# Kernel tuning notes

Hardware: AMD Instinct MI355X
Metric: run time of the kernel (lower is better)

The kernel has to match this reference:

```python
import jax, jax.numpy as jnp
import numpy as np
from jax import lax

FIR_TAPS = np.array([1.0, 3.0, 3.0, 1.0], dtype=np.float32)
FACTOR = 2
GAIN = 1.0


def _fir_kernel(C):
    # _setup_kernel: outer product, normalize to sum 1; upsample scales by gain*factor**2
    k = np.outer(FIR_TAPS, FIR_TAPS)
    k = k / k.sum() * (GAIN * FACTOR ** 2)  # 4x4 kernel, sum == 4
    k = jnp.asarray(k, jnp.float32)
    return jnp.tile(k[None, None], (C, 1, 1, 1))  # [C,1,4,4] depthwise


def setup_inputs() -> dict:
    key = jax.random.key(0)
    k1, k2, k3 = jax.random.split(key, 3)
    x = jax.random.normal(k1, (16, 256, 64, 64), jnp.float32)
    W = jax.random.normal(k2, (256, 256, 3, 3), jnp.float32) * 0.02
    b = jax.random.normal(k3, (256,), jnp.float32) * 0.02
    return {"x": x, "W": W, "b": b}


def reference(x, W, b):
    B, C, H, Wd = x.shape
    kern = _fir_kernel(C)
    # upfirdn2d upsample: zero-insert by 2 (lhs_dilation), pad0=2 / pad1=1(+up-1=2),
    # depthwise FIR correlation -> [B, C, 2H, 2W]
    p0, p1 = 2, 2  # pad1 = p//2 + (factor-1) trailing zeros folded into padding
    h = lax.conv_general_dilated(
        x, kern, window_strides=(1, 1), padding=((p0, p1), (p0, p1)),
        lhs_dilation=(FACTOR, FACTOR),
        dimension_numbers=("NCHW", "OIHW", "NCHW"), feature_group_count=C)
    # 3x3 conv, padding=1, stride=1 -> [B, out_ch, 2H, 2W]
    y = lax.conv_general_dilated(
        h, W, window_strides=(1, 1), padding=((1, 1), (1, 1)),
        dimension_numbers=("NCHW", "OIHW", "NCHW"))
    return y + b[None, :, None, None]
```

## Files before the change

### kernel.cpp

```cpp
#include <hip/hip_runtime.h>
#include <hip/hip_bf16.h>
#include <stdint.h>

typedef __attribute__((ext_vector_type(8))) short bf16x8;
typedef __attribute__((ext_vector_type(4))) float f32x4;

#define PH 130
#define NT 36
#define ITERS 18

__device__ __forceinline__ short f2bf(float f) {
  uint32_t u = __builtin_bit_cast(uint32_t, f);
  u = (u + 0x7FFFu + ((u >> 16) & 1u)) >> 16;
  return (short)u;
}

__device__ __forceinline__ void gload16(const void* g, void* l) {
  __builtin_amdgcn_global_load_lds(
      (const __attribute__((address_space(1))) void*)g,
      (__attribute__((address_space(3))) void*)l, 16, 0, 0);
}

__global__ void wpack(const float* __restrict__ W, short* __restrict__ A) {
  int tid = blockIdx.x * 256 + threadIdx.x;
  if (tid >= 256 * 2304) return;
  int co = tid / 2304;
  int r  = tid - co * 2304;
  int tap = r >> 8, ci = r & 255;
  A[tid] = f2bf(W[((size_t)(co * 256 + ci)) * 9 + tap]);
}

__global__ void fir_up(const float* __restrict__ x, short* __restrict__ hT) {
  const int bp = blockIdx.x;
  const int b = bp / PH, pp = bp - b * PH;
  const int ci0 = blockIdx.y << 6;
  const int t = threadIdx.x;
  short* outrow = hT + ((size_t)(b * PH + pp) * PH) * 256 + ci0;

  if (pp == 0 || pp == PH - 1) {
    for (int idx = t; idx < PH * 64; idx += 256) {
      int qp = idx >> 6, c = idx & 63;
      outrow[(size_t)qp * 256 + c] = 0;
    }
    return;
  }
  const int p = pp - 1;
  int i0, i1; float wr0, wr1;
  if (!(p & 1)) { i0 = (p >> 1) - 1; i1 = p >> 1;     wr0 = 0.25f; wr1 = 0.75f; }
  else          { i0 = p >> 1;       i1 = (p >> 1)+1; wr0 = 0.75f; wr1 = 0.25f; }

  __shared__ float X[2][64][65];
#pragma unroll
  for (int r = 0; r < 2; ++r) {
    int ir = r ? i1 : i0;
    bool ok = (ir >= 0 && ir < 64);
#pragma unroll
    for (int it = 0; it < 4; ++it) {
      int idx = it * 256 + t;
      int ci = idx >> 4, jq = idx & 15;
      f32x4 v = {0.f, 0.f, 0.f, 0.f};
      if (ok)
        v = *(const f32x4*)&x[((size_t)(b * 256 + ci0 + ci) * 64 + ir) * 64 + jq * 4];
      X[r][jq * 4 + 0][ci] = v[0];
      X[r][jq * 4 + 1][ci] = v[1];
      X[r][jq * 4 + 2][ci] = v[2];
      X[r][jq * 4 + 3][ci] = v[3];
    }
  }
  __syncthreads();

  const int c = t & 63;
  for (int qp = (t >> 6); qp < PH; qp += 4) {
    float val = 0.f;
    if (qp >= 1 && qp <= 128) {
      int q = qp - 1;
      int j0, j1; float wc0, wc1;
      if (!(q & 1)) { j0 = (q >> 1) - 1; j1 = q >> 1; wc0 = 0.25f; wc1 = 0.75f; }
      else          { j0 = q >> 1;       j1 = j0 + 1; wc0 = 0.75f; wc1 = 0.25f; }
      float v00 = (j0 >= 0) ? X[0][j0][c] : 0.f;
      float v10 = (j0 >= 0) ? X[1][j0][c] : 0.f;
      float v01 = (j1 < 64) ? X[0][j1][c] : 0.f;
      float v11 = (j1 < 64) ? X[1][j1][c] : 0.f;
      val = wr0 * (wc0 * v00 + wc1 * v01) + wr1 * (wc0 * v10 + wc1 * v11);
    }
    outrow[(size_t)qp * 256 + c] = f2bf(val);
  }
}

__global__ __launch_bounds__(512) void conv3x3_gemm(
    const short* __restrict__ hT, const short* __restrict__ Wp,
    const float* __restrict__ bias, float* __restrict__ y) {
  __shared__ short ldsA[2][16384];
  __shared__ short ldsB[2][16384];
  const int tid = threadIdx.x;
  const int lane = tid & 63, w = tid >> 6;
  const int wm = w >> 2, wn = w & 3;

  const int bid = blockIdx.x;
  const int jblk = (bid & 7) * 32 + (bid >> 3);

  int aRow[4], aKk[4];
  const short* srcB[4];
#pragma unroll
  for (int h = 0; h < 2; ++h)
#pragma unroll
    for (int i = 0; i < 2; ++i) {
      int o = h * 16384 + i * 8192 + w * 1024 + lane * 16;
      int L = o ^ (((o >> 7) & 7) << 4);
      int row = L >> 7, kk = (L & 127) >> 1;
      aRow[h * 2 + i] = row; aKk[h * 2 + i] = kk;
      srcB[h * 2 + i] = Wp + (size_t)row * 2304 + kk;
    }

  int aP[2], bP[2];
#pragma unroll
  for (int ks = 0; ks < 2; ++ks) {
    int La = (wm * 128 + (lane & 15)) * 128 + (lane >> 4) * 16 + ks * 64;
    aP[ks] = La ^ ((lane & 7) << 4);
    int Lb = (wn * 64 + (lane & 15)) * 128 + (lane >> 4) * 16 + ks * 64;
    bP[ks] = Lb ^ ((lane & 7) << 4);
  }

  const char* LA0 = (const char*)&ldsA[0][0];
  const char* LB0 = (const char*)&ldsB[0][0];
  const char* LA1 = (const char*)&ldsA[1][0];
  const char* LB1 = (const char*)&ldsB[1][0];

  for (int mi = 0; mi < 4; ++mi) {
    const int tau = jblk * 4 + mi;
    const int b = tau >> 6, p0 = (tau & 63) * 2;

    const short* srcA[4];
#pragma unroll
    for (int j = 0; j < 4; ++j)
      srcA[j] = hT + ((size_t)((b * PH + p0 + (aRow[j] >> 7)) * PH + (aRow[j] & 127))) * 256 + aKk[j];

    auto offA = [&](int t) {
      int tap = t >> 2, ci0 = (t & 3) << 6;
      int dm = (tap >= 6) ? 2 : (tap >= 3) ? 1 : 0;
      int dn = tap - 3 * dm;
      return (dm * PH + dn) * 256 + ci0;
    };
    auto offB = [&](int t) { return (t >> 2) * 256 + ((t & 3) << 6); };

    auto stageA = [&](int t, int h) {
      int o = offA(t);
      short* dst = &ldsA[t & 1][h * 8192];
#pragma unroll
      for (int i = 0; i < 2; ++i)
        gload16(srcA[h * 2 + i] + o, dst + i * 4096 + w * 512);
    };
    auto stageB = [&](int t, int h) {
      int o = offB(t);
      short* dst = &ldsB[t & 1][h * 8192];
#pragma unroll
      for (int i = 0; i < 2; ++i)
        gload16(srcB[h * 2 + i] + o, dst + i * 4096 + w * 512);
    };

    stageA(0, 0); stageB(0, 0); stageB(0, 1); stageA(0, 1);
    stageA(1, 0); stageB(1, 0); stageB(1, 1);
    asm volatile("s_waitcnt vmcnt(6)" ::: "memory");
    __builtin_amdgcn_s_barrier();

    f32x4 acc[8][4];
#pragma unroll
    for (int m = 0; m < 8; ++m)
#pragma unroll
      for (int n = 0; n < 4; ++n) acc[m][n] = (f32x4){0.f, 0.f, 0.f, 0.f};

    for (int i = 0; i < ITERS; ++i) {
      const int u = 2 * i, v = u + 1;
      const bool more = (u + 2 < NT);
      bf16x8 a_[2][4], c_[2][4], b_[2][2], b2[2][2];

#pragma unroll
      for (int ks = 0; ks < 2; ++ks) {
#pragma unroll
        for (int m = 0; m < 4; ++m) a_[ks][m] = *(const bf16x8*)(LA0 + aP[ks] + m * 2048);
#pragma unroll
        for (int n = 0; n < 2; ++n) b_[ks][n] = *(const bf16x8*)(LB0 + bP[ks] + n * 2048);
      }
      stageA(v, 1);
      asm volatile("s_waitcnt lgkmcnt(8)" ::: "memory");
      __builtin_amdgcn_s_barrier();
      asm volatile("s_waitcnt lgkmcnt(0)" ::: "memory");
      __builtin_amdgcn_s_setprio(1);
#pragma unroll
      for (int m = 0; m < 4; ++m)
#pragma unroll
        for (int n = 0; n < 2; ++n) {
          acc[m][n] = __builtin_amdgcn_mfma_f32_16x16x32_bf16(a_[0][m], b_[0][n], acc[m][n], 0, 0, 0);
          acc[m][n] = __builtin_amdgcn_mfma_f32_16x16x32_bf16(a_[1][m], b_[1][n], acc[m][n], 0, 0, 0);
        }
      __builtin_amdgcn_s_setprio(0);
      __builtin_amdgcn_s_barrier();

#pragma unroll
      for (int ks = 0; ks < 2; ++ks)
#pragma unroll
        for (int n = 0; n < 2; ++n) b2[ks][n] = *(const bf16x8*)(LB0 + bP[ks] + (n + 2) * 2048);
      __builtin_amdgcn_s_barrier();
      asm volatile("s_waitcnt lgkmcnt(0)" ::: "memory");
      __builtin_amdgcn_s_setprio(1);
#pragma unroll
      for (int m = 0; m < 4; ++m)
#pragma unroll
        for (int n = 0; n < 2; ++n) {
          acc[m][n + 2] = __builtin_amdgcn_mfma_f32_16x16x32_bf16(a_[0][m], b2[0][n], acc[m][n + 2], 0, 0, 0);
          acc[m][n + 2] = __builtin_amdgcn_mfma_f32_16x16x32_bf16(a_[1][m], b2[1][n], acc[m][n + 2], 0, 0, 0);
        }
      __builtin_amdgcn_s_setprio(0);
      __builtin_amdgcn_s_barrier();

#pragma unroll
      for (int ks = 0; ks < 2; ++ks)
#pragma unroll
        for (int m = 0; m < 4; ++m) c_[ks][m] = *(const bf16x8*)(LA0 + aP[ks] + (m + 4) * 2048);
      if (more) stageB(u + 2, 0);
      __builtin_amdgcn_s_barrier();
      asm volatile("s_waitcnt lgkmcnt(0)" ::: "memory");
      __builtin_amdgcn_s_setprio(1);
#pragma unroll
      for (int m = 0; m < 4; ++m)
#pragma unroll
        for (int n = 0; n < 2; ++n) {
          acc[m + 4][n] = __builtin_amdgcn_mfma_f32_16x16x32_bf16(c_[0][m], b_[0][n], acc[m + 4][n], 0, 0, 0);
          acc[m + 4][n] = __builtin_amdgcn_mfma_f32_16x16x32_bf16(c_[1][m], b_[1][n], acc[m + 4][n], 0, 0, 0);
        }
      __builtin_amdgcn_s_setprio(0);
      __builtin_amdgcn_s_barrier();

      if (more) { stageB(u + 2, 1); stageA(u + 2, 0); }
      __builtin_amdgcn_s_barrier();
      __builtin_amdgcn_s_setprio(1);
#pragma unroll
      for (int m = 0; m < 4; ++m)
#pragma unroll
        for (int n = 0; n < 2; ++n) {
          acc[m + 4][n + 2] = __builtin_amdgcn_mfma_f32_16x16x32_bf16(c_[0][m], b2[0][n], acc[m + 4][n + 2], 0, 0, 0);
          acc[m + 4][n + 2] = __builtin_amdgcn_mfma_f32_16x16x32_bf16(c_[1][m], b2[1][n], acc[m + 4][n + 2], 0, 0, 0);
        }
      __builtin_amdgcn_s_setprio(0);
      if (more) asm volatile("s_waitcnt vmcnt(6)" ::: "memory");
      else      asm volatile("s_waitcnt vmcnt(0)" ::: "memory");
      __builtin_amdgcn_s_barrier();

#pragma unroll
      for (int ks = 0; ks < 2; ++ks) {
#pragma unroll
        for (int m = 0; m < 4; ++m) a_[ks][m] = *(const bf16x8*)(LA1 + aP[ks] + m * 2048);
#pragma unroll
        for (int n = 0; n < 2; ++n) b_[ks][n] = *(const bf16x8*)(LB1 + bP[ks] + n * 2048);
      }
      if (more) stageA(u + 2, 1);
      asm volatile("s_waitcnt lgkmcnt(8)" ::: "memory");
      __builtin_amdgcn_s_barrier();
      asm volatile("s_waitcnt lgkmcnt(0)" ::: "memory");
      __builtin_amdgcn_s_setprio(1);
#pragma unroll
      for (int m = 0; m < 4; ++m)
#pragma unroll
        for (int n = 0; n < 2; ++n) {
          acc[m][n] = __builtin_amdgcn_mfma_f32_16x16x32_bf16(a_[0][m], b_[0][n], acc[m][n], 0, 0, 0);
          acc[m][n] = __builtin_amdgcn_mfma_f32_16x16x32_bf16(a_[1][m], b_[1][n], acc[m][n], 0, 0, 0);
        }
      __builtin_amdgcn_s_setprio(0);
      __builtin_amdgcn_s_barrier();

#pragma unroll
      for (int ks = 0; ks < 2; ++ks)
#pragma unroll
        for (int n = 0; n < 2; ++n) b2[ks][n] = *(const bf16x8*)(LB1 + bP[ks] + (n + 2) * 2048);
      __builtin_amdgcn_s_barrier();
      asm volatile("s_waitcnt lgkmcnt(0)" ::: "memory");
      __builtin_amdgcn_s_setprio(1);
#pragma unroll
      for (int m = 0; m < 4; ++m)
#pragma unroll
        for (int n = 0; n < 2; ++n) {
          acc[m][n + 2] = __builtin_amdgcn_mfma_f32_16x16x32_bf16(a_[0][m], b2[0][n], acc[m][n + 2], 0, 0, 0);
          acc[m][n + 2] = __builtin_amdgcn_mfma_f32_16x16x32_bf16(a_[1][m], b2[1][n], acc[m][n + 2], 0, 0, 0);
        }
      __builtin_amdgcn_s_setprio(0);
      __builtin_amdgcn_s_barrier();

#pragma unroll
      for (int ks = 0; ks < 2; ++ks)
#pragma unroll
        for (int m = 0; m < 4; ++m) c_[ks][m] = *(const bf16x8*)(LA1 + aP[ks] + (m + 4) * 2048);
      if (more) stageB(u + 3, 0);
      __builtin_amdgcn_s_barrier();
      asm volatile("s_waitcnt lgkmcnt(0)" ::: "memory");
      __builtin_amdgcn_s_setprio(1);
#pragma unroll
      for (int m = 0; m < 4; ++m)
#pragma unroll
        for (int n = 0; n < 2; ++n) {
          acc[m + 4][n] = __builtin_amdgcn_mfma_f32_16x16x32_bf16(c_[0][m], b_[0][n], acc[m + 4][n], 0, 0, 0);
          acc[m + 4][n] = __builtin_amdgcn_mfma_f32_16x16x32_bf16(c_[1][m], b_[1][n], acc[m + 4][n], 0, 0, 0);
        }
      __builtin_amdgcn_s_setprio(0);
      __builtin_amdgcn_s_barrier();

      if (more) { stageB(u + 3, 1); stageA(u + 3, 0); }
      __builtin_amdgcn_s_barrier();
      __builtin_amdgcn_s_setprio(1);
#pragma unroll
      for (int m = 0; m < 4; ++m)
#pragma unroll
        for (int n = 0; n < 2; ++n) {
          acc[m + 4][n + 2] = __builtin_amdgcn_mfma_f32_16x16x32_bf16(c_[0][m], b2[0][n], acc[m + 4][n + 2], 0, 0, 0);
          acc[m + 4][n + 2] = __builtin_amdgcn_mfma_f32_16x16x32_bf16(c_[1][m], b2[1][n], acc[m + 4][n + 2], 0, 0, 0);
        }
      __builtin_amdgcn_s_setprio(0);
      if (more) asm volatile("s_waitcnt vmcnt(6)" ::: "memory");
      __builtin_amdgcn_s_barrier();
    }

#pragma unroll
    for (int n = 0; n < 4; ++n) {
      int co = wn * 64 + n * 16 + (lane & 15);
      float bv = bias[co];
      float* yp = y + (((size_t)(b * 256 + co)) * 128 + (p0 + wm)) * 128;
#pragma unroll
      for (int m = 0; m < 8; ++m) {
        int q0 = m * 16 + ((lane >> 4) << 2);
        f32x4 vv = acc[m][n];
        vv[0] += bv; vv[1] += bv; vv[2] += bv; vv[3] += bv;
        *(f32x4*)(yp + q0) = vv;
      }
    }
  }
}

extern "C" void kernel_launch(void* const* d_in, const int* in_sizes, int n_in,
                              void* d_out, int out_size, void* d_ws, size_t ws_size,
                              hipStream_t stream) {
  const float* x    = (const float*)d_in[0];
  const float* W    = (const float*)d_in[1];
  const float* bias = (const float*)d_in[2];
  float* y = (float*)d_out;

  const size_t hT_bytes = (size_t)16 * PH * PH * 256 * 2;
  const size_t A_bytes  = (size_t)256 * 2304 * 2;
  if (ws_size < hT_bytes + A_bytes) return;

  short* hT = (short*)d_ws;
  short* Wp = (short*)((char*)d_ws + hT_bytes);

  wpack<<<(256 * 2304 + 255) / 256, 256, 0, stream>>>(W, Wp);
  dim3 g1(16 * PH, 4);
  fir_up<<<g1, 256, 0, stream>>>(x, hT);
  conv3x3_gemm<<<256, 512, 0, stream>>>(hT, Wp, bias, y);
}
```

Measured before the change: 431.2 us.

## Launch one GEMM tile per block and separate the FIR upsample into row then column passes

After: 390.6 us. 1.1x faster.

```diff
diff --git a/kernel.cpp b/kernel.cpp
--- a/kernel.cpp
+++ b/kernel.cpp
@@ -13,6 +13,10 @@
   uint32_t u = __builtin_bit_cast(uint32_t, f);
   u = (u + 0x7FFFu + ((u >> 16) & 1u)) >> 16;
   return (short)u;
+}
+
+__device__ __forceinline__ uint32_t pack2bf(float lo, float hi) {
+  return ((uint32_t)(uint16_t)f2bf(hi) << 16) | (uint16_t)f2bf(lo);
 }
 
 __device__ __forceinline__ void gload16(const void* g, void* l) {
@@ -38,9 +42,9 @@
   short* outrow = hT + ((size_t)(b * PH + pp) * PH) * 256 + ci0;
 
   if (pp == 0 || pp == PH - 1) {
-    for (int idx = t; idx < PH * 64; idx += 256) {
-      int qp = idx >> 6, c = idx & 63;
-      outrow[(size_t)qp * 256 + c] = 0;
+    for (int idx = t; idx < PH * 32; idx += 256) {
+      int qp = idx >> 5, c2 = idx & 31;
+      *(uint32_t*)&outrow[(size_t)qp * 256 + c2 * 2] = 0u;
     }
     return;
   }
@@ -69,21 +73,33 @@
   }
   __syncthreads();
 
-  const int c = t & 63;
-  for (int qp = (t >> 6); qp < PH; qp += 4) {
-    float val = 0.f;
+  {
+    float* base = &X[0][0][0];
+#pragma unroll
+    for (int it = 0; it < 16; ++it) {
+      int idx = it * 256 + t;
+      int a = idx + (idx >> 6);
+      base[a] = wr0 * base[a] + wr1 * base[a + 64 * 65];
+    }
+  }
+  __syncthreads();
+
+  const int c2 = (t & 31) * 2;
+  const int qg = t >> 5;
+  for (int qp = qg; qp < PH; qp += 8) {
+    uint32_t out = 0u;
     if (qp >= 1 && qp <= 128) {
       int q = qp - 1;
-      int j0, j1; float wc0, wc1;
-      if (!(q & 1)) { j0 = (q >> 1) - 1; j1 = q >> 1; wc0 = 0.25f; wc1 = 0.75f; }
-      else          { j0 = q >> 1;       j1 = j0 + 1; wc0 = 0.75f; wc1 = 0.25f; }
-      float v00 = (j0 >= 0) ? X[0][j0][c] : 0.f;
-      float v10 = (j0 >= 0) ? X[1][j0][c] : 0.f;
-      float v01 = (j1 < 64) ? X[0][j1][c] : 0.f;
-      float v11 = (j1 < 64) ? X[1][j1][c] : 0.f;
-      val = wr0 * (wc0 * v00 + wc1 * v01) + wr1 * (wc0 * v10 + wc1 * v11);
-    }
-    outrow[(size_t)qp * 256 + c] = f2bf(val);
+      int par = q & 1;
+      int jb = (q >> 1) - 1 + par;
+      float wc0 = par ? 0.75f : 0.25f;
+      float wc1 = par ? 0.25f : 0.75f;
+      float v00 = 0.f, v01 = 0.f, v10 = 0.f, v11 = 0.f;
+      if (jb >= 0)     { v00 = X[0][jb][c2];     v01 = X[0][jb][c2 + 1]; }
+      if (jb + 1 < 64) { v10 = X[0][jb + 1][c2]; v11 = X[0][jb + 1][c2 + 1]; }
+      out = pack2bf(wc0 * v00 + wc1 * v10, wc0 * v01 + wc1 * v11);
+    }
+    *(uint32_t*)&outrow[(size_t)qp * 256 + c2] = out;
   }
 }
 
@@ -97,9 +113,10 @@
   const int wm = w >> 2, wn = w & 3;
 
   const int bid = blockIdx.x;
-  const int jblk = (bid & 7) * 32 + (bid >> 3);
-
-  int aRow[4], aKk[4];
+  const int tau = (bid & 7) * 128 + (bid >> 3);
+  const int b = tau >> 6, p0 = (tau & 63) * 2;
+
+  const short* srcA[4];
   const short* srcB[4];
 #pragma unroll
   for (int h = 0; h < 2; ++h)
@@ -108,9 +125,32 @@
       int o = h * 16384 + i * 8192 + w * 1024 + lane * 16;
       int L = o ^ (((o >> 7) & 7) << 4);
       int row = L >> 7, kk = (L & 127) >> 1;
-      aRow[h * 2 + i] = row; aKk[h * 2 + i] = kk;
+      srcA[h * 2 + i] = hT + ((size_t)((b * PH + p0 + (row >> 7)) * PH + (row & 127))) * 256 + kk;
       srcB[h * 2 + i] = Wp + (size_t)row * 2304 + kk;
     }
+
+  auto offA = [&](int t) {
+    int tap = t >> 2, ci0 = (t & 3) << 6;
+    int dm = (tap >= 6) ? 2 : (tap >= 3) ? 1 : 0;
+    int dn = tap - 3 * dm;
+    return (dm * PH + dn) * 256 + ci0;
+  };
+  auto offB = [&](int t) { return (t >> 2) * 256 + ((t & 3) << 6); };
+
+  auto stageA = [&](int t, int h) {
+    int o = offA(t);
+    short* dst = &ldsA[t & 1][h * 8192];
+#pragma unroll
+    for (int i = 0; i < 2; ++i)
+      gload16(srcA[h * 2 + i] + o, dst + i * 4096 + w * 512);
+  };
+  auto stageB = [&](int t, int h) {
+    int o = offB(t);
+    short* dst = &ldsB[t & 1][h * 8192];
+#pragma unroll
+    for (int i = 0; i < 2; ++i)
+      gload16(srcB[h * 2 + i] + o, dst + i * 4096 + w * 512);
+  };
 
   int aP[2], bP[2];
 #pragma unroll
@@ -126,210 +166,175 @@
   const char* LA1 = (const char*)&ldsA[1][0];
   const char* LB1 = (const char*)&ldsB[1][0];
 
-  for (int mi = 0; mi < 4; ++mi) {
-    const int tau = jblk * 4 + mi;
-    const int b = tau >> 6, p0 = (tau & 63) * 2;
-
-    const short* srcA[4];
-#pragma unroll
-    for (int j = 0; j < 4; ++j)
-      srcA[j] = hT + ((size_t)((b * PH + p0 + (aRow[j] >> 7)) * PH + (aRow[j] & 127))) * 256 + aKk[j];
-
-    auto offA = [&](int t) {
-      int tap = t >> 2, ci0 = (t & 3) << 6;
-      int dm = (tap >= 6) ? 2 : (tap >= 3) ? 1 : 0;
-      int dn = tap - 3 * dm;
-      return (dm * PH + dn) * 256 + ci0;
-    };
-    auto offB = [&](int t) { return (t >> 2) * 256 + ((t & 3) << 6); };
-
-    auto stageA = [&](int t, int h) {
-      int o = offA(t);
-      short* dst = &ldsA[t & 1][h * 8192];
-#pragma unroll
-      for (int i = 0; i < 2; ++i)
-        gload16(srcA[h * 2 + i] + o, dst + i * 4096 + w * 512);
-    };
-    auto stageB = [&](int t, int h) {
-      int o = offB(t);
-      short* dst = &ldsB[t & 1][h * 8192];
-#pragma unroll
-      for (int i = 0; i < 2; ++i)
-        gload16(srcB[h * 2 + i] + o, dst + i * 4096 + w * 512);
-    };
-
-    stageA(0, 0); stageB(0, 0); stageB(0, 1); stageA(0, 1);
-    stageA(1, 0); stageB(1, 0); stageB(1, 1);
-    asm volatile("s_waitcnt vmcnt(6)" ::: "memory");
-    __builtin_amdgcn_s_barrier();
-
-    f32x4 acc[8][4];
-#pragma unroll
-    for (int m = 0; m < 8; ++m)
-#pragma unroll
-      for (int n = 0; n < 4; ++n) acc[m][n] = (f32x4){0.f, 0.f, 0.f, 0.f};
-
-    for (int i = 0; i < ITERS; ++i) {
-      const int u = 2 * i, v = u + 1;
-      const bool more = (u + 2 < NT);
-      bf16x8 a_[2][4], c_[2][4], b_[2][2], b2[2][2];
-
-#pragma unroll
-      for (int ks = 0; ks < 2; ++ks) {
-#pragma unroll
-        for (int m = 0; m < 4; ++m) a_[ks][m] = *(const bf16x8*)(LA0 + aP[ks] + m * 2048);
-#pragma unroll
-        for (int n = 0; n < 2; ++n) b_[ks][n] = *(const bf16x8*)(LB0 + bP[ks] + n * 2048);
-      }
-      stageA(v, 1);
-      asm volatile("s_waitcnt lgkmcnt(8)" ::: "memory");
-      __builtin_amdgcn_s_barrier();
-      asm volatile("s_waitcnt lgkmcnt(0)" ::: "memory");
-      __builtin_amdgcn_s_setprio(1);
-#pragma unroll
-      for (int m = 0; m < 4; ++m)
-#pragma unroll
-        for (int n = 0; n < 2; ++n) {
-          acc[m][n] = __builtin_amdgcn_mfma_f32_16x16x32_bf16(a_[0][m], b_[0][n], acc[m][n], 0, 0, 0);
-          acc[m][n] = __builtin_amdgcn_mfma_f32_16x16x32_bf16(a_[1][m], b_[1][n], acc[m][n], 0, 0, 0);
-        }
-      __builtin_amdgcn_s_setprio(0);
-      __builtin_amdgcn_s_barrier();
-
-#pragma unroll
-      for (int ks = 0; ks < 2; ++ks)
-#pragma unroll
-        for (int n = 0; n < 2; ++n) b2[ks][n] = *(const bf16x8*)(LB0 + bP[ks] + (n + 2) * 2048);
-      __builtin_amdgcn_s_barrier();
-      asm volatile("s_waitcnt lgkmcnt(0)" ::: "memory");
-      __builtin_amdgcn_s_setprio(1);
-#pragma unroll
-      for (int m = 0; m < 4; ++m)
-#pragma unroll
-        for (int n = 0; n < 2; ++n) {
-          acc[m][n + 2] = __builtin_amdgcn_mfma_f32_16x16x32_bf16(a_[0][m], b2[0][n], acc[m][n + 2], 0, 0, 0);
-          acc[m][n + 2] = __builtin_amdgcn_mfma_f32_16x16x32_bf16(a_[1][m], b2[1][n], acc[m][n + 2], 0, 0, 0);
-        }
-      __builtin_amdgcn_s_setprio(0);
-      __builtin_amdgcn_s_barrier();
-
-#pragma unroll
-      for (int ks = 0; ks < 2; ++ks)
-#pragma unroll
-        for (int m = 0; m < 4; ++m) c_[ks][m] = *(const bf16x8*)(LA0 + aP[ks] + (m + 4) * 2048);
-      if (more) stageB(u + 2, 0);
-      __builtin_amdgcn_s_barrier();
-      asm volatile("s_waitcnt lgkmcnt(0)" ::: "memory");
-      __builtin_amdgcn_s_setprio(1);
-#pragma unroll
-      for (int m = 0; m < 4; ++m)
-#pragma unroll
-        for (int n = 0; n < 2; ++n) {
-          acc[m + 4][n] = __builtin_amdgcn_mfma_f32_16x16x32_bf16(c_[0][m], b_[0][n], acc[m + 4][n], 0, 0, 0);
-          acc[m + 4][n] = __builtin_amdgcn_mfma_f32_16x16x32_bf16(c_[1][m], b_[1][n], acc[m + 4][n], 0, 0, 0);
-        }
-      __builtin_amdgcn_s_setprio(0);
-      __builtin_amdgcn_s_barrier();
-
-      if (more) { stageB(u + 2, 1); stageA(u + 2, 0); }
-      __builtin_amdgcn_s_barrier();
-      __builtin_amdgcn_s_setprio(1);
-#pragma unroll
-      for (int m = 0; m < 4; ++m)
-#pragma unroll
-        for (int n = 0; n < 2; ++n) {
-          acc[m + 4][n + 2] = __builtin_amdgcn_mfma_f32_16x16x32_bf16(c_[0][m], b2[0][n], acc[m + 4][n + 2], 0, 0, 0);
-          acc[m + 4][n + 2] = __builtin_amdgcn_mfma_f32_16x16x32_bf16(c_[1][m], b2[1][n], acc[m + 4][n + 2], 0, 0, 0);
-        }
-      __builtin_amdgcn_s_setprio(0);
-      if (more) asm volatile("s_waitcnt vmcnt(6)" ::: "memory");
-      else      asm volatile("s_waitcnt vmcnt(0)" ::: "memory");
-      __builtin_amdgcn_s_barrier();
-
-#pragma unroll
-      for (int ks = 0; ks < 2; ++ks) {
-#pragma unroll
-        for (int m = 0; m < 4; ++m) a_[ks][m] = *(const bf16x8*)(LA1 + aP[ks] + m * 2048);
-#pragma unroll
-        for (int n = 0; n < 2; ++n) b_[ks][n] = *(const bf16x8*)(LB1 + bP[ks] + n * 2048);
-      }
-      if (more) stageA(u + 2, 1);
-      asm volatile("s_waitcnt lgkmcnt(8)" ::: "memory");
-      __builtin_amdgcn_s_barrier();
-      asm volatile("s_waitcnt lgkmcnt(0)" ::: "memory");
-      __builtin_amdgcn_s_setprio(1);
-#pragma unroll
-      for (int m = 0; m < 4; ++m)
-#pragma unroll
-        for (int n = 0; n < 2; ++n) {
-          acc[m][n] = __builtin_amdgcn_mfma_f32_16x16x32_bf16(a_[0][m], b_[0][n], acc[m][n], 0, 0, 0);
-          acc[m][n] = __builtin_amdgcn_mfma_f32_16x16x32_bf16(a_[1][m], b_[1][n], acc[m][n], 0, 0, 0);
-        }
-      __builtin_amdgcn_s_setprio(0);
-      __builtin_amdgcn_s_barrier();
-
-#pragma unroll
-      for (int ks = 0; ks < 2; ++ks)
-#pragma unroll
-        for (int n = 0; n < 2; ++n) b2[ks][n] = *(const bf16x8*)(LB1 + bP[ks] + (n + 2) * 2048);
-      __builtin_amdgcn_s_barrier();
-      asm volatile("s_waitcnt lgkmcnt(0)" ::: "memory");
-      __builtin_amdgcn_s_setprio(1);
-#pragma unroll
-      for (int m = 0; m < 4; ++m)
-#pragma unroll
-        for (int n = 0; n < 2; ++n) {
-          acc[m][n + 2] = __builtin_amdgcn_mfma_f32_16x16x32_bf16(a_[0][m], b2[0][n], acc[m][n + 2], 0, 0, 0);
-          acc[m][n + 2] = __builtin_amdgcn_mfma_f32_16x16x32_bf16(a_[1][m], b2[1][n], acc[m][n + 2], 0, 0, 0);
-        }
-      __builtin_amdgcn_s_setprio(0);
-      __builtin_amdgcn_s_barrier();
-
-#pragma unroll
-      for (int ks = 0; ks < 2; ++ks)
-#pragma unroll
-        for (int m = 0; m < 4; ++m) c_[ks][m] = *(const bf16x8*)(LA1 + aP[ks] + (m + 4) * 2048);
-      if (more) stageB(u + 3, 0);
-      __builtin_amdgcn_s_barrier();
-      asm volatile("s_waitcnt lgkmcnt(0)" ::: "memory");
-      __builtin_amdgcn_s_setprio(1);
-#pragma unroll
-      for (int m = 0; m < 4; ++m)
-#pragma unroll
-        for (int n = 0; n < 2; ++n) {
-          acc[m + 4][n] = __builtin_amdgcn_mfma_f32_16x16x32_bf16(c_[0][m], b_[0][n], acc[m + 4][n], 0, 0, 0);
-          acc[m + 4][n] = __builtin_amdgcn_mfma_f32_16x16x32_bf16(c_[1][m], b_[1][n], acc[m + 4][n], 0, 0, 0);
-        }
-      __builtin_amdgcn_s_setprio(0);
-      __builtin_amdgcn_s_barrier();
-
-      if (more) { stageB(u + 3, 1); stageA(u + 3, 0); }
-      __builtin_amdgcn_s_barrier();
-      __builtin_amdgcn_s_setprio(1);
-#pragma unroll
-      for (int m = 0; m < 4; ++m)
-#pragma unroll
-        for (int n = 0; n < 2; ++n) {
-          acc[m + 4][n + 2] = __builtin_amdgcn_mfma_f32_16x16x32_bf16(c_[0][m], b2[0][n], acc[m + 4][n + 2], 0, 0, 0);
-          acc[m + 4][n + 2] = __builtin_amdgcn_mfma_f32_16x16x32_bf16(c_[1][m], b2[1][n], acc[m + 4][n + 2], 0, 0, 0);
-        }
-      __builtin_amdgcn_s_setprio(0);
-      if (more) asm volatile("s_waitcnt vmcnt(6)" ::: "memory");
-      __builtin_amdgcn_s_barrier();
-    }
-
-#pragma unroll
-    for (int n = 0; n < 4; ++n) {
-      int co = wn * 64 + n * 16 + (lane & 15);
-      float bv = bias[co];
-      float* yp = y + (((size_t)(b * 256 + co)) * 128 + (p0 + wm)) * 128;
-#pragma unroll
-      for (int m = 0; m < 8; ++m) {
-        int q0 = m * 16 + ((lane >> 4) << 2);
-        f32x4 vv = acc[m][n];
-        vv[0] += bv; vv[1] += bv; vv[2] += bv; vv[3] += bv;
-        *(f32x4*)(yp + q0) = vv;
-      }
+  stageA(0, 0); stageB(0, 0); stageB(0, 1); stageA(0, 1);
+  stageA(1, 0); stageB(1, 0); stageB(1, 1);
+  asm volatile("s_waitcnt vmcnt(6)" ::: "memory");
+  __builtin_amdgcn_s_barrier();
+
+  f32x4 acc[8][4];
+#pragma unroll
+  for (int m = 0; m < 8; ++m)
+#pragma unroll
+    for (int n = 0; n < 4; ++n) acc[m][n] = (f32x4){0.f, 0.f, 0.f, 0.f};
+
+  for (int i = 0; i < ITERS; ++i) {
+    const int u = 2 * i, v = u + 1;
+    const bool more = (u + 2 < NT);
+    bf16x8 a_[2][4], c_[2][4], b_[2][2], b2[2][2];
+
+#pragma unroll
+    for (int ks = 0; ks < 2; ++ks) {
+#pragma unroll
+      for (int m = 0; m < 4; ++m) a_[ks][m] = *(const bf16x8*)(LA0 + aP[ks] + m * 2048);
+#pragma unroll
+      for (int n = 0; n < 2; ++n) b_[ks][n] = *(const bf16x8*)(LB0 + bP[ks] + n * 2048);
+    }
+    stageA(v, 1);
+    __builtin_amdgcn_s_barrier();
+    asm volatile("s_waitcnt lgkmcnt(0)" ::: "memory");
+    __builtin_amdgcn_s_setprio(1);
+#pragma unroll
+    for (int m = 0; m < 4; ++m)
+#pragma unroll
+      for (int n = 0; n < 2; ++n) {
+        acc[m][n] = __builtin_amdgcn_mfma_f32_16x16x32_bf16(a_[0][m], b_[0][n], acc[m][n], 0, 0, 0);
+        acc[m][n] = __builtin_amdgcn_mfma_f32_16x16x32_bf16(a_[1][m], b_[1][n], acc[m][n], 0, 0, 0);
+      }
+    __builtin_amdgcn_s_setprio(0);
+    __builtin_amdgcn_s_barrier();
+
+#pragma unroll
+    for (int ks = 0; ks < 2; ++ks)
+#pragma unroll
+      for (int n = 0; n < 2; ++n) b2[ks][n] = *(const bf16x8*)(LB0 + bP[ks] + (n + 2) * 2048);
+    __builtin_amdgcn_s_barrier();
+    asm volatile("s_waitcnt lgkmcnt(0)" ::: "memory");
+    __builtin_amdgcn_s_setprio(1);
+#pragma unroll
+    for (int m = 0; m < 4; ++m)
+#pragma unroll
+      for (int n = 0; n < 2; ++n) {
+        acc[m][n + 2] = __builtin_amdgcn_mfma_f32_16x16x32_bf16(a_[0][m], b2[0][n], acc[m][n + 2], 0, 0, 0);
+        acc[m][n + 2] = __builtin_amdgcn_mfma_f32_16x16x32_bf16(a_[1][m], b2[1][n], acc[m][n + 2], 0, 0, 0);
+      }
+    __builtin_amdgcn_s_setprio(0);
+    __builtin_amdgcn_s_barrier();
+
+#pragma unroll
+    for (int ks = 0; ks < 2; ++ks)
+#pragma unroll
+      for (int m = 0; m < 4; ++m) c_[ks][m] = *(const bf16x8*)(LA0 + aP[ks] + (m + 4) * 2048);
+    if (more) stageB(u + 2, 0);
+    __builtin_amdgcn_s_barrier();
+    asm volatile("s_waitcnt lgkmcnt(0)" ::: "memory");
+    __builtin_amdgcn_s_setprio(1);
+#pragma unroll
+    for (int m = 0; m < 4; ++m)
+#pragma unroll
+      for (int n = 0; n < 2; ++n) {
+        acc[m + 4][n] = __builtin_amdgcn_mfma_f32_16x16x32_bf16(c_[0][m], b_[0][n], acc[m + 4][n], 0, 0, 0);
+        acc[m + 4][n] = __builtin_amdgcn_mfma_f32_16x16x32_bf16(c_[1][m], b_[1][n], acc[m + 4][n], 0, 0, 0);
+      }
+    __builtin_amdgcn_s_setprio(0);
+    __builtin_amdgcn_s_barrier();
+
+    if (more) { stageB(u + 2, 1); stageA(u + 2, 0); }
+    __builtin_amdgcn_s_barrier();
+    __builtin_amdgcn_s_setprio(1);
+#pragma unroll
+    for (int m = 0; m < 4; ++m)
+#pragma unroll
+      for (int n = 0; n < 2; ++n) {
+        acc[m + 4][n + 2] = __builtin_amdgcn_mfma_f32_16x16x32_bf16(c_[0][m], b2[0][n], acc[m + 4][n + 2], 0, 0, 0);
+        acc[m + 4][n + 2] = __builtin_amdgcn_mfma_f32_16x16x32_bf16(c_[1][m], b2[1][n], acc[m + 4][n + 2], 0, 0, 0);
+      }
+    __builtin_amdgcn_s_setprio(0);
+    if (more) asm volatile("s_waitcnt vmcnt(6)" ::: "memory");
+    else      asm volatile("s_waitcnt vmcnt(0)" ::: "memory");
+    __builtin_amdgcn_s_barrier();
+
+#pragma unroll
+    for (int ks = 0; ks < 2; ++ks) {
+#pragma unroll
+      for (int m = 0; m < 4; ++m) a_[ks][m] = *(const bf16x8*)(LA1 + aP[ks] + m * 2048);
+#pragma unroll
+      for (int n = 0; n < 2; ++n) b_[ks][n] = *(const bf16x8*)(LB1 + bP[ks] + n * 2048);
+    }
+    if (more) stageA(u + 2, 1);
+    __builtin_amdgcn_s_barrier();
+    asm volatile("s_waitcnt lgkmcnt(0)" ::: "memory");
+    __builtin_amdgcn_s_setprio(1);
+#pragma unroll
+    for (int m = 0; m < 4; ++m)
+#pragma unroll
+      for (int n = 0; n < 2; ++n) {
+        acc[m][n] = __builtin_amdgcn_mfma_f32_16x16x32_bf16(a_[0][m], b_[0][n], acc[m][n], 0, 0, 0);
+        acc[m][n] = __builtin_amdgcn_mfma_f32_16x16x32_bf16(a_[1][m], b_[1][n], acc[m][n], 0, 0, 0);
+      }
+    __builtin_amdgcn_s_setprio(0);
+    __builtin_amdgcn_s_barrier();
+
+#pragma unroll
+    for (int ks = 0; ks < 2; ++ks)
+#pragma unroll
+      for (int n = 0; n < 2; ++n) b2[ks][n] = *(const bf16x8*)(LB1 + bP[ks] + (n + 2) * 2048);
+    __builtin_amdgcn_s_barrier();
+    asm volatile("s_waitcnt lgkmcnt(0)" ::: "memory");
+    __builtin_amdgcn_s_setprio(1);
+#pragma unroll
+    for (int m = 0; m < 4; ++m)
+#pragma unroll
+      for (int n = 0; n < 2; ++n) {
+        acc[m][n + 2] = __builtin_amdgcn_mfma_f32_16x16x32_bf16(a_[0][m], b2[0][n], acc[m][n + 2], 0, 0, 0);
+        acc[m][n + 2] = __builtin_amdgcn_mfma_f32_16x16x32_bf16(a_[1][m], b2[1][n], acc[m][n + 2], 0, 0, 0);
+      }
+    __builtin_amdgcn_s_setprio(0);
+    __builtin_amdgcn_s_barrier();
+
+#pragma unroll
+    for (int ks = 0; ks < 2; ++ks)
+#pragma unroll
+      for (int m = 0; m < 4; ++m) c_[ks][m] = *(const bf16x8*)(LA1 + aP[ks] + (m + 4) * 2048);
+    if (more) stageB(u + 3, 0);
+    __builtin_amdgcn_s_barrier();
+    asm volatile("s_waitcnt lgkmcnt(0)" ::: "memory");
+    __builtin_amdgcn_s_setprio(1);
+#pragma unroll
+    for (int m = 0; m < 4; ++m)
+#pragma unroll
+      for (int n = 0; n < 2; ++n) {
+        acc[m + 4][n] = __builtin_amdgcn_mfma_f32_16x16x32_bf16(c_[0][m], b_[0][n], acc[m + 4][n], 0, 0, 0);
+        acc[m + 4][n] = __builtin_amdgcn_mfma_f32_16x16x32_bf16(c_[1][m], b_[1][n], acc[m + 4][n], 0, 0, 0);
+      }
+    __builtin_amdgcn_s_setprio(0);
+    __builtin_amdgcn_s_barrier();
+
+    if (more) { stageB(u + 3, 1); stageA(u + 3, 0); }
+    __builtin_amdgcn_s_barrier();
+    __builtin_amdgcn_s_setprio(1);
+#pragma unroll
+    for (int m = 0; m < 4; ++m)
+#pragma unroll
+      for (int n = 0; n < 2; ++n) {
+        acc[m + 4][n + 2] = __builtin_amdgcn_mfma_f32_16x16x32_bf16(c_[0][m], b2[0][n], acc[m + 4][n + 2], 0, 0, 0);
+        acc[m + 4][n + 2] = __builtin_amdgcn_mfma_f32_16x16x32_bf16(c_[1][m], b2[1][n], acc[m + 4][n + 2], 0, 0, 0);
+      }
+    __builtin_amdgcn_s_setprio(0);
+    if (more) asm volatile("s_waitcnt vmcnt(6)" ::: "memory");
+    __builtin_amdgcn_s_barrier();
+  }
+
+#pragma unroll
+  for (int n = 0; n < 4; ++n) {
+    int co = wn * 64 + n * 16 + (lane & 15);
+    float bv = bias[co];
+    float* yp = y + (((size_t)(b * 256 + co)) * 128 + (p0 + wm)) * 128;
+#pragma unroll
+    for (int m = 0; m < 8; ++m) {
+      int q0 = m * 16 + ((lane >> 4) << 2);
+      f32x4 vv = acc[m][n];
+      vv[0] += bv; vv[1] += bv; vv[2] += bv; vv[3] += bv;
+      *(f32x4*)(yp + q0) = vv;
     }
   }
 }
@@ -352,5 +357,5 @@
   wpack<<<(256 * 2304 + 255) / 256, 256, 0, stream>>>(W, Wp);
   dim3 g1(16 * PH, 4);
   fir_up<<<g1, 256, 0, stream>>>(x, hT);
-  conv3x3_gemm<<<256, 512, 0, stream>>>(hT, Wp, bias, y);
-}
+  conv3x3_gemm<<<1024, 512, 0, stream>>>(hT, Wp, bias, y);
+}
```
